# Optimization experiments

Hardware: AMD Instinct MI355X
Metric: run time of the kernel (lower is better)

Reference implementation:

```python
import jax, jax.numpy as jnp
import numpy as np
from jax import lax

DN = ('NCHW', 'OIHW', 'NCHW')

def _conv(x, w, b):
    y = lax.conv_general_dilated(x, w, (1, 1), 'SAME', dimension_numbers=DN)
    return y + b[None, :, None, None]

def setup_inputs() -> dict:
    key = jax.random.key(0)
    ks = jax.random.split(key, 11)
    B, C, H, W = 8, 16, 64, 64
    hid, K = 128, 8192
    s = 0.02
    return {
        'x': jax.random.normal(ks[0], (B, C, H, W), jnp.float32),
        # encoder: Conv2d(C->hid,3x3), GELU, Conv2d(hid->hid,3x3), GELU
        'ew1': jax.random.normal(ks[1], (hid, C, 3, 3), jnp.float32) * s,
        'eb1': jnp.zeros((hid,), jnp.float32),
        'ew2': jax.random.normal(ks[2], (hid, hid, 3, 3), jnp.float32) * s,
        'eb2': jnp.zeros((hid,), jnp.float32),
        # codebook: Embedding(K, hid), init normal std=0.02
        'embed': jax.random.normal(ks[3], (K, hid), jnp.float32) * s,
        # decoder: Conv2d(hid->hid,3x3), GELU, Conv2d(hid->C,1x1), sigmoid
        'dw1': jax.random.normal(ks[4], (hid, hid, 3, 3), jnp.float32) * s,
        'db1': jnp.zeros((hid,), jnp.float32),
        'dw2': jax.random.normal(ks[5], (C, hid, 1, 1), jnp.float32) * s,
        'db2': jnp.zeros((C,), jnp.float32),
    }

def reference(x, ew1, eb1, ew2, eb2, embed, dw1, db1, dw2, db2):
    # --- encoder ---
    h = jax.nn.gelu(_conv(x, ew1, eb1), approximate=False)
    h = jax.nn.gelu(_conv(h, ew2, eb2), approximate=False)  # [B, D, H, W]
    B, D, H, W = h.shape
    flat = jnp.transpose(h, (0, 2, 3, 1)).reshape(B * H * W, D)  # [N, D]
    # --- VQ: pairwise sq-dist + argmin (no_grad in original) ---
    flat_ng = lax.stop_gradient(flat)
    d2 = (jnp.sum(flat_ng * flat_ng, axis=1, keepdims=True)
          - 2.0 * flat_ng @ embed.T
          + jnp.sum(embed * embed, axis=1)[None, :])  # [N, K]
    idx = jnp.argmin(d2, axis=1)  # [N]
    z = idx.reshape(B, H, W)
    q = embed[idx].reshape(B, H, W, D)  # gather
    # --- decoder ---
    qc = jnp.transpose(q, (0, 3, 1, 2))  # NCHW
    y = jax.nn.gelu(_conv(qc, dw1, db1), approximate=False)
    x_hat = jax.nn.sigmoid(_conv(y, dw2, db2))  # [B, C, H, W]
    return x_hat
```

## Files before the change

kernel.cpp:

```cpp
#include <hip/hip_runtime.h>

constexpr int B_ = 8, H_ = 64, W_ = 64, C0 = 16, D_ = 128, K_ = 8192;
constexpr int N_ = B_ * H_ * W_;

typedef __attribute__((ext_vector_type(8))) short short8;
typedef __attribute__((ext_vector_type(4))) float f32x4;

__device__ __forceinline__ float gelu_f(float x) {
    return 0.5f * x * (1.0f + erff(x * 0.70710678118654752440f));
}

__device__ __forceinline__ unsigned short f2bf(float f) {
    unsigned u = __float_as_uint(f);
    u += 0x7fffu + ((u >> 16) & 1u);
    return (unsigned short)(u >> 16);
}

__device__ __forceinline__ void gload_lds16(const void* g, void* l) {
    __builtin_amdgcn_global_load_lds(
        (const __attribute__((address_space(1))) unsigned int*)g,
        (__attribute__((address_space(3))) unsigned int*)l, 16, 0, 0);
}

__global__ __launch_bounds__(256) void prep_kernel(
    const float* __restrict__ x, const float* __restrict__ ew1,
    const float* __restrict__ ew2, const float* __restrict__ dw1,
    const float* __restrict__ embed, unsigned short* __restrict__ xtbf,
    unsigned short* __restrict__ wtbf2, unsigned short* __restrict__ wtbf3,
    float* __restrict__ e2n, unsigned short* __restrict__ embbf,
    unsigned short* __restrict__ wtb1b,
    unsigned long long* __restrict__ partial,
    unsigned short* __restrict__ embq) {
    int blk = blockIdx.x;
    int tid = threadIdx.x;
    if (blk < 2048) {
        int j = blk * 256 + tid;
        int c = j & 15, w = (j >> 4) & 63, h = (j >> 10) & 63, b = j >> 16;
        xtbf[j] = f2bf(x[(((b << 4) + c) << 12) + (h << 6) + w]);
    } else if (blk < 3200) {
        const float* src = (blk < 2624) ? ew2 : dw1;
        unsigned short* dst = (blk < 2624) ? wtbf2 : wtbf3;
        int i = (blk - ((blk < 2624) ? 2048 : 2624)) * 256 + tid;
        int ci = i & 127, co = (i >> 7) & 127, t = i >> 14;
        dst[i] = f2bf(src[(co * 128 + ci) * 9 + t]);
    } else if (blk < 3232) {
        int k = (blk - 3200) * 256 + tid;
        const float4* e4 = (const float4*)(embed + (size_t)k * 128);
        float s = 0.0f;
#pragma unroll 8
        for (int i = 0; i < 32; ++i) {
            float4 v = e4[i];
            s += v.x * v.x + v.y * v.y + v.z * v.z + v.w * v.w;
        }
        e2n[k] = -0.5f * s;
    } else if (blk < 4256) {
        int i = (blk - 3232) * 256 + tid;
        float4 v = ((const float4*)embed)[i];
        uint2 o;
        o.x = (unsigned)f2bf(v.x) | ((unsigned)f2bf(v.y) << 16);
        o.y = (unsigned)f2bf(v.z) | ((unsigned)f2bf(v.w) << 16);
        ((uint2*)embbf)[i] = o;
    } else if (blk < 4336) {
        int i = (blk - 4256) * 256 + tid;
        int co = i / 160, kk = i % 160;
        float v = 0.0f;
        if (kk < 144) {
            int t = kk >> 4, ci = kk & 15;
            v = ew1[(co * 16 + ci) * 9 + t];
        }
        wtb1b[i] = f2bf(v);
    } else if (blk < 4464) {
        int i = (blk - 4336) * 256 + tid;
        partial[i] = 0ULL;
    } else {
        int s = (blk - 4464) * 256 + tid;
        int T = s >> 10;
        int rem = s & 1023;
        int kk = rem >> 8, nsp = (rem >> 6) & 3, q = (rem >> 4) & 3,
            r = rem & 15;
        int code = T * 64 + nsp * 16 + r;
        int d0 = kk * 32 + q * 8;
        const float* ep = embed + (size_t)code * 128 + d0;
        unsigned short* op = embq + (size_t)s * 8;
#pragma unroll
        for (int e = 0; e < 8; ++e) op[e] = f2bf(ep[e]);
    }
}

__global__ __launch_bounds__(256, 2) void conv1_mfma_kernel(
    const unsigned short* __restrict__ xtbf,
    const unsigned short* __restrict__ wtb1b,
    const float* __restrict__ bias,
    unsigned short* __restrict__ out) {
    constexpr int LDA = 168;
    __shared__ __align__(16) unsigned short As[64 * LDA];
    int tid = threadIdx.x;
    int wv = tid >> 6, lane = tid & 63;
    int r = lane & 15, q = lane >> 4;
    int h0 = blockIdx.x & 63, b = blockIdx.x >> 6;

    short8 bf1[5][2];
#pragma unroll
    for (int k = 0; k < 5; ++k)
#pragma unroll
        for (int ns = 0; ns < 2; ++ns)
            bf1[k][ns] = *(const short8*)(wtb1b + (wv * 32 + ns * 16 + r) * 160 +
                                          k * 32 + q * 8);

#pragma unroll
    for (int j = 0; j < 5; ++j) {
        int s = tid + j * 256;
        if (s < 1152) {
            int px = s / 18, rem = s % 18;
            int t = rem >> 1, half = rem & 1;
            int hh = h0 + t / 3 - 1, ww = px + t % 3 - 1;
            float4 v = make_float4(0.f, 0.f, 0.f, 0.f);
            if ((unsigned)hh < 64u && (unsigned)ww < 64u)
                v = *(const float4*)(xtbf + (((b * 64 + hh) * 64 + ww) << 4) +
                                     half * 8);
            *(float4*)(As + px * LDA + t * 16 + half * 8) = v;
        } else {
            int z = s - 1152;
            int px = z >> 1, half = z & 1;
            *(float4*)(As + px * LDA + 144 + half * 8) =
                make_float4(0.f, 0.f, 0.f, 0.f);
        }
    }
    __syncthreads();

    f32x4 acc[4][2];
#pragma unroll
    for (int ms = 0; ms < 4; ++ms)
#pragma unroll
        for (int ns = 0; ns < 2; ++ns) acc[ms][ns] = (f32x4){0.f, 0.f, 0.f, 0.f};

#pragma unroll
    for (int k = 0; k < 5; ++k) {
        short8 af[4];
#pragma unroll
        for (int ms = 0; ms < 4; ++ms)
            af[ms] = *(const short8*)(As + (ms * 16 + r) * LDA + k * 32 + q * 8);
#pragma unroll
        for (int ms = 0; ms < 4; ++ms)
#pragma unroll
            for (int ns = 0; ns < 2; ++ns)
                acc[ms][ns] = __builtin_amdgcn_mfma_f32_16x16x32_bf16(
                    af[ms], bf1[k][ns], acc[ms][ns], 0, 0, 0);
    }

#pragma unroll
    for (int ns = 0; ns < 2; ++ns) {
        int co = wv * 32 + ns * 16 + r;
        float bv = bias[co];
#pragma unroll
        for (int ms = 0; ms < 4; ++ms)
#pragma unroll
            for (int rg = 0; rg < 4; ++rg) {
                int px = ms * 16 + q * 4 + rg;
                int pix = (b * 64 + h0) * 64 + px;
                out[(size_t)pix * 128 + co] = f2bf(gelu_f(acc[ms][ns][rg] + bv));
            }
    }
}

template <bool OUT_BF16, bool GATHER, bool FUSE>
__global__ __launch_bounds__(256, 2) void conv3x3_mfma_kernel(
    const unsigned short* __restrict__ in,
    const unsigned long long* __restrict__ gidx,
    const unsigned short* __restrict__ wtb,
    const float* __restrict__ bias,
    const float* __restrict__ w2,
    const float* __restrict__ b2,
    void* __restrict__ out_) {
    constexpr int LDC = 136;
    __shared__ __align__(16) unsigned short As[3 * 66 * LDC];
    __shared__ __align__(16) float ws2[FUSE ? 2048 : 4];
    int tid = threadIdx.x;
    int wv = tid >> 6, lane = tid & 63;
    int r = lane & 15, q = lane >> 4;
    int h0 = blockIdx.x & 63, b = blockIdx.x >> 6;

    constexpr int NJ = FUSE ? 15 : 13;
    for (int j = 0; j < NJ; ++j) {
        int s = tid + j * 256;
        if (s < 3168) {
            int col = s >> 4, chunk = s & 15;
            int ry = col / 66, cx = col % 66;
            int hh = h0 - 1 + ry, ww = cx - 1;
            float4 v = make_float4(0.f, 0.f, 0.f, 0.f);
            if ((unsigned)hh < 64u && (unsigned)ww < 64u) {
                int pix = (b * 64 + hh) * 64 + ww;
                const unsigned short* src;
                if (GATHER) {
                    int k = 8191 - (int)(unsigned)(gidx[pix] & 0xFFFFFFFFu);
                    src = in + (size_t)k * 128;
                } else {
                    src = in + (size_t)pix * 128;
                }
                v = *(const float4*)(src + chunk * 8);
            }
            *(float4*)(As + col * LDC + chunk * 8) = v;
        } else if (FUSE && s < 3680) {
            int i = s - 3168;
            ((float4*)ws2)[i] = ((const float4*)w2)[i];
        }
    }
    __syncthreads();

    f32x4 acc[4][2];
#pragma unroll
    for (int ms = 0; ms < 4; ++ms)
#pragma unroll
        for (int ns = 0; ns < 2; ++ns) acc[ms][ns] = (f32x4){0.f, 0.f, 0.f, 0.f};

    const unsigned short* wbase = wtb + (wv * 32 + r) * 128 + q * 8;
    short8 bfp[2][2];
    bfp[0][0] = *(const short8*)(wbase);
    bfp[0][1] = *(const short8*)(wbase + 2048);
    int gcur = 0;
    for (int t = 0; t < 9; ++t) {
        int dy = t / 3, dx = t % 3;
#pragma unroll
        for (int k = 0; k < 4; ++k) {
            int cur = gcur & 1, nxt = cur ^ 1;
            if (gcur < 35) {
                int g1 = gcur + 1;
                int t1 = g1 >> 2, k1 = g1 & 3;
                const unsigned short* wp = wbase + t1 * 16384 + k1 * 32;
                bfp[nxt][0] = *(const short8*)(wp);
                bfp[nxt][1] = *(const short8*)(wp + 2048);
            }
            short8 af[4];
#pragma unroll
            for (int ms = 0; ms < 4; ++ms) {
                int col = dy * 66 + ms * 16 + r + dx;
                af[ms] = *(const short8*)(As + col * LDC + k * 32 + q * 8);
            }
#pragma unroll
            for (int ms = 0; ms < 4; ++ms)
#pragma unroll
                for (int ns = 0; ns < 2; ++ns)
                    acc[ms][ns] = __builtin_amdgcn_mfma_f32_16x16x32_bf16(
                        af[ms], bfp[cur][ns], acc[ms][ns], 0, 0, 0);
            ++gcur;
        }
    }

    if (!FUSE) {
#pragma unroll
        for (int ns = 0; ns < 2; ++ns) {
            int co = wv * 32 + ns * 16 + r;
            float bv = bias[co];
#pragma unroll
            for (int ms = 0; ms < 4; ++ms)
#pragma unroll
                for (int rg = 0; rg < 4; ++rg) {
                    int px = ms * 16 + q * 4 + rg;
                    int pix = (b * 64 + h0) * 64 + px;
                    float g = gelu_f(acc[ms][ns][rg] + bv);
                    if (OUT_BF16)
                        ((unsigned short*)out_)[(size_t)pix * 128 + co] = f2bf(g);
                    else
                        ((float*)out_)[(size_t)pix * 128 + co] = g;
                }
        }
    } else {
        __syncthreads();
        float* gbuf = (float*)As;
#pragma unroll
        for (int ns = 0; ns < 2; ++ns) {
            int co = wv * 32 + ns * 16 + r;
            float bv = bias[co];
#pragma unroll
            for (int ms = 0; ms < 4; ++ms)
#pragma unroll
                for (int rg = 0; rg < 4; ++rg) {
                    int px = ms * 16 + q * 4 + rg;
                    gbuf[px * 130 + co] = gelu_f(acc[ms][ns][rg] + bv);
                }
        }
        __syncthreads();
        int w_ = tid & 63, c0 = (tid >> 6) * 4;
        float a4[4] = {b2[c0], b2[c0 + 1], b2[c0 + 2], b2[c0 + 3]};
#pragma unroll 1
        for (int ci = 0; ci < 128; ci += 2) {
            float2 yv = *(const float2*)&gbuf[w_ * 130 + ci];
#pragma unroll
            for (int jc = 0; jc < 4; ++jc) {
                float2 wv2 = *(const float2*)&ws2[(c0 + jc) * 128 + ci];
                a4[jc] += yv.x * wv2.x + yv.y * wv2.y;
            }
        }
        float* outp = (float*)out_;
#pragma unroll
        for (int jc = 0; jc < 4; ++jc) {
            float v = 1.0f / (1.0f + expf(-a4[jc]));
            outp[(((size_t)b * 16 + c0 + jc) * 64 + h0) * 64 + w_] = v;
        }
    }
}

__global__ __launch_bounds__(256, 2) void vq_mfma_kernel(
    const unsigned short* __restrict__ flatbf,
    const unsigned short* __restrict__ embq,
    const float* __restrict__ e2n,
    unsigned long long* __restrict__ partial) {
    __shared__ __align__(16) unsigned short Bs[2][8192];
    int tid = threadIdx.x;
    int wv = tid >> 6, lane = tid & 63;
    int r = lane & 15, q = lane >> 4;
    int p_h = wv & 1;
    int c_s = wv >> 1;
    int half = blockIdx.x & 1;
    int m0 = (blockIdx.x >> 1) * 64;
    int kbase = half * 4096;
    int t0 = half * 64;

    short8 af[4][2];
#pragma unroll
    for (int kk = 0; kk < 4; ++kk)
#pragma unroll
        for (int ms = 0; ms < 2; ++ms)
            af[kk][ms] = *(const short8*)(
                flatbf + (size_t)(m0 + p_h * 32 + ms * 16 + r) * 128 +
                kk * 32 + q * 8);

    const float* e2p = e2n + kbase + c_s * 32 + r;
    float e2a = e2p[0], e2b = e2p[16];
    float e2nx0 = 0.f, e2nx1 = 0.f;

    {
        const unsigned short* src = embq + (size_t)t0 * 8192;
#pragma unroll
        for (int j = 0; j < 4; ++j) {
            int o = (j * 4 + wv) * 512;
            gload_lds16(src + o + lane * 8, &Bs[0][o]);
        }
    }

    float best[2][4];
#pragma unroll
    for (int ms = 0; ms < 2; ++ms)
#pragma unroll
        for (int rg = 0; rg < 4; ++rg) best[ms][rg] = -3.4e38f;

    __syncthreads();

    f32x4 acc[2][2];
#pragma unroll
    for (int ms = 0; ms < 2; ++ms) {
        acc[ms][0] = (f32x4){e2a, e2a, e2a, e2a};
        acc[ms][1] = (f32x4){e2b, e2b, e2b, e2b};
    }

    int cur = 0;
#pragma unroll 1
    for (int it = 0; it < 64; ++it) {
        if (it < 63) {
            const unsigned short* src = embq + (size_t)(t0 + it + 1) * 8192;
            unsigned short* dst = &Bs[cur ^ 1][0];
#pragma unroll
            for (int j = 0; j < 4; ++j) {
                int o = (j * 4 + wv) * 512;
                gload_lds16(src + o + lane * 8, dst + o);
            }
            e2nx0 = e2p[(it + 1) * 64];
            e2nx1 = e2p[(it + 1) * 64 + 16];
        }
        const unsigned short* bb = &Bs[cur][0];
#pragma unroll
        for (int kk = 0; kk < 4; ++kk) {
            short8 bf0 = *(const short8*)(bb + kk * 2048 + (c_s * 2) * 512 +
                                          q * 128 + r * 8);
            short8 bf1 = *(const short8*)(bb + kk * 2048 + (c_s * 2 + 1) * 512 +
                                          q * 128 + r * 8);
#pragma unroll
            for (int ms = 0; ms < 2; ++ms) {
                acc[ms][0] = __builtin_amdgcn_mfma_f32_16x16x32_bf16(
                    af[kk][ms], bf0, acc[ms][0], 0, 0, 0);
                acc[ms][1] = __builtin_amdgcn_mfma_f32_16x16x32_bf16(
                    af[kk][ms], bf1, acc[ms][1], 0, 0, 0);
            }
        }
        unsigned kb = (unsigned)(2047 - ((it & 31) * 64 + c_s * 32 + r));
#pragma unroll
        for (int ms = 0; ms < 2; ++ms)
#pragma unroll
            for (int rg = 0; rg < 4; ++rg) {
                float u0 = __uint_as_float(
                    (__float_as_uint(acc[ms][0][rg]) & 0xFFFFF800u) | kb);
                float u1 = __uint_as_float(
                    (__float_as_uint(acc[ms][1][rg]) & 0xFFFFF800u) |
                    (kb - 16u));
                best[ms][rg] = fmaxf(best[ms][rg], fmaxf(u0, u1));
            }
        if ((it & 31) == 31) {
#pragma unroll
            for (int ms = 0; ms < 2; ++ms)
#pragma unroll
                for (int rg = 0; rg < 4; ++rg) {
                    float v = best[ms][rg];
#pragma unroll
                    for (int m = 1; m < 16; m <<= 1)
                        v = fmaxf(v, __shfl_xor(v, m));
                    if (r == 0) {
                        unsigned bits = __float_as_uint(v);
                        int cand = 2047 - (int)(bits & 2047u);
                        int code = kbase + (it >> 5) * 2048 + cand;
                        unsigned sb = (bits & 0x80000000u) ? ~bits
                                                           : (bits | 0x80000000u);
                        unsigned long long packed =
                            ((unsigned long long)sb << 32) |
                            (unsigned)(8191 - code);
                        atomicMax(
                            partial + m0 + p_h * 32 + ms * 16 + q * 4 + rg,
                            packed);
                    }
                    best[ms][rg] = -3.4e38f;
                }
        }
        if (it < 63) {
#pragma unroll
            for (int ms = 0; ms < 2; ++ms) {
                acc[ms][0] = (f32x4){e2nx0, e2nx0, e2nx0, e2nx0};
                acc[ms][1] = (f32x4){e2nx1, e2nx1, e2nx1, e2nx1};
            }
        }
        __syncthreads();
        cur ^= 1;
    }
}

extern "C" void kernel_launch(void* const* d_in, const int* in_sizes, int n_in,
                              void* d_out, int out_size, void* d_ws,
                              size_t ws_size, hipStream_t stream) {
    const float* x = (const float*)d_in[0];
    const float* ew1 = (const float*)d_in[1];
    const float* eb1 = (const float*)d_in[2];
    const float* ew2 = (const float*)d_in[3];
    const float* eb2 = (const float*)d_in[4];
    const float* embed = (const float*)d_in[5];
    const float* dw1 = (const float*)d_in[6];
    const float* db1 = (const float*)d_in[7];
    const float* dw2 = (const float*)d_in[8];
    const float* db2 = (const float*)d_in[9];
    float* out = (float*)d_out;

    float* e2n = (float*)d_ws;
    unsigned long long* partial =
        (unsigned long long*)(e2n + 8192);
    unsigned short* xtbf = (unsigned short*)(partial + 32768);
    unsigned short* wtb1b = xtbf + 524288;
    unsigned short* wtbf2 = wtb1b + 20480;
    unsigned short* wtbf3 = wtbf2 + 147456;
    unsigned short* embbf = wtbf3 + 147456;
    unsigned short* abf = embbf + 1048576;
    unsigned short* flatbf = abf + 4194304;
    unsigned short* embq = flatbf + 4194304;

    prep_kernel<<<4976, 256, 0, stream>>>(x, ew1, ew2, dw1, embed, xtbf, wtbf2,
                                          wtbf3, e2n, embbf, wtb1b, partial,
                                          embq);
    conv1_mfma_kernel<<<512, 256, 0, stream>>>(xtbf, wtb1b, eb1, abf);
    conv3x3_mfma_kernel<true, false, false><<<512, 256, 0, stream>>>(
        abf, nullptr, wtbf2, eb2, nullptr, nullptr, flatbf);
    vq_mfma_kernel<<<1024, 256, 0, stream>>>(flatbf, embq, e2n, partial);
    conv3x3_mfma_kernel<false, true, true><<<512, 256, 0, stream>>>(
        embbf, partial, wtbf3, db1, dw2, db2, out);
}
```

Measured before the change: 222.7 us.

## Split 3x3 convs across output-channel halves and unfuse 1x1 decoder conv

The 3x3 conv kernels now launch twice as many blocks, each computing 64 output channels instead of 128. Each wave preloads all 36 of its weight fragments into registers instead of double-buffering them from global memory. The fused 1x1 conv and sigmoid epilogue moves into a separate dec2_kernel, which reads an fp32 intermediate written to workspace. This raises parallelism and removes weight-load latency from the MMA loop. In exchange, each input tile is loaded twice, register use rises, and an extra global round-trip for the fp32 intermediate plus an extra launch are added.

```diff
diff --git a/kernel.cpp b/kernel.cpp
--- a/kernel.cpp
+++ b/kernel.cpp
@@ -163,25 +163,31 @@
     }
 }
 
-template <bool OUT_BF16, bool GATHER, bool FUSE>
-__global__ __launch_bounds__(256, 2) void conv3x3_mfma_kernel(
+template <bool GATHER, bool OUT_F32>
+__global__ __launch_bounds__(256, 2) void conv3x3_w64_kernel(
     const unsigned short* __restrict__ in,
     const unsigned long long* __restrict__ gidx,
     const unsigned short* __restrict__ wtb,
     const float* __restrict__ bias,
-    const float* __restrict__ w2,
-    const float* __restrict__ b2,
     void* __restrict__ out_) {
     constexpr int LDC = 136;
     __shared__ __align__(16) unsigned short As[3 * 66 * LDC];
-    __shared__ __align__(16) float ws2[FUSE ? 2048 : 4];
     int tid = threadIdx.x;
     int wv = tid >> 6, lane = tid & 63;
     int r = lane & 15, q = lane >> 4;
-    int h0 = blockIdx.x & 63, b = blockIdx.x >> 6;
-
-    constexpr int NJ = FUSE ? 15 : 13;
-    for (int j = 0; j < NJ; ++j) {
+    int h0 = blockIdx.x & 63, b = (blockIdx.x >> 6) & 7;
+    int coh = blockIdx.x >> 9;
+    int co = coh * 64 + wv * 16 + r;
+
+    short8 wfr[9][4];
+#pragma unroll
+    for (int t = 0; t < 9; ++t)
+#pragma unroll
+        for (int k = 0; k < 4; ++k)
+            wfr[t][k] = *(const short8*)(wtb + t * 16384 + co * 128 + k * 32 +
+                                         q * 8);
+
+    for (int j = 0; j < 13; ++j) {
         int s = tid + j * 256;
         if (s < 3168) {
             int col = s >> 4, chunk = s & 15;
@@ -200,36 +206,19 @@
                 v = *(const float4*)(src + chunk * 8);
             }
             *(float4*)(As + col * LDC + chunk * 8) = v;
-        } else if (FUSE && s < 3680) {
-            int i = s - 3168;
-            ((float4*)ws2)[i] = ((const float4*)w2)[i];
         }
     }
     __syncthreads();
 
-    f32x4 acc[4][2];
-#pragma unroll
-    for (int ms = 0; ms < 4; ++ms)
-#pragma unroll
-        for (int ns = 0; ns < 2; ++ns) acc[ms][ns] = (f32x4){0.f, 0.f, 0.f, 0.f};
-
-    const unsigned short* wbase = wtb + (wv * 32 + r) * 128 + q * 8;
-    short8 bfp[2][2];
-    bfp[0][0] = *(const short8*)(wbase);
-    bfp[0][1] = *(const short8*)(wbase + 2048);
-    int gcur = 0;
+    f32x4 acc[4];
+#pragma unroll
+    for (int ms = 0; ms < 4; ++ms) acc[ms] = (f32x4){0.f, 0.f, 0.f, 0.f};
+
+#pragma unroll
     for (int t = 0; t < 9; ++t) {
         int dy = t / 3, dx = t % 3;
 #pragma unroll
         for (int k = 0; k < 4; ++k) {
-            int cur = gcur & 1, nxt = cur ^ 1;
-            if (gcur < 35) {
-                int g1 = gcur + 1;
-                int t1 = g1 >> 2, k1 = g1 & 3;
-                const unsigned short* wp = wbase + t1 * 16384 + k1 * 32;
-                bfp[nxt][0] = *(const short8*)(wp);
-                bfp[nxt][1] = *(const short8*)(wp + 2048);
-            }
             short8 af[4];
 #pragma unroll
             for (int ms = 0; ms < 4; ++ms) {
@@ -238,65 +227,63 @@
             }
 #pragma unroll
             for (int ms = 0; ms < 4; ++ms)
-#pragma unroll
-                for (int ns = 0; ns < 2; ++ns)
-                    acc[ms][ns] = __builtin_amdgcn_mfma_f32_16x16x32_bf16(
-                        af[ms], bfp[cur][ns], acc[ms][ns], 0, 0, 0);
-            ++gcur;
-        }
-    }
-
-    if (!FUSE) {
-#pragma unroll
-        for (int ns = 0; ns < 2; ++ns) {
-            int co = wv * 32 + ns * 16 + r;
-            float bv = bias[co];
-#pragma unroll
-            for (int ms = 0; ms < 4; ++ms)
-#pragma unroll
-                for (int rg = 0; rg < 4; ++rg) {
-                    int px = ms * 16 + q * 4 + rg;
-                    int pix = (b * 64 + h0) * 64 + px;
-                    float g = gelu_f(acc[ms][ns][rg] + bv);
-                    if (OUT_BF16)
-                        ((unsigned short*)out_)[(size_t)pix * 128 + co] = f2bf(g);
-                    else
-                        ((float*)out_)[(size_t)pix * 128 + co] = g;
-                }
-        }
-    } else {
-        __syncthreads();
-        float* gbuf = (float*)As;
-#pragma unroll
-        for (int ns = 0; ns < 2; ++ns) {
-            int co = wv * 32 + ns * 16 + r;
-            float bv = bias[co];
-#pragma unroll
-            for (int ms = 0; ms < 4; ++ms)
-#pragma unroll
-                for (int rg = 0; rg < 4; ++rg) {
-                    int px = ms * 16 + q * 4 + rg;
-                    gbuf[px * 130 + co] = gelu_f(acc[ms][ns][rg] + bv);
-                }
-        }
-        __syncthreads();
-        int w_ = tid & 63, c0 = (tid >> 6) * 4;
-        float a4[4] = {b2[c0], b2[c0 + 1], b2[c0 + 2], b2[c0 + 3]};
+                acc[ms] = __builtin_amdgcn_mfma_f32_16x16x32_bf16(
+                    af[ms], wfr[t][k], acc[ms], 0, 0, 0);
+        }
+    }
+
+    float bv = bias[co];
+#pragma unroll
+    for (int ms = 0; ms < 4; ++ms)
+#pragma unroll
+        for (int rg = 0; rg < 4; ++rg) {
+            int px = ms * 16 + q * 4 + rg;
+            int pix = (b * 64 + h0) * 64 + px;
+            float g = gelu_f(acc[ms][rg] + bv);
+            if (OUT_F32)
+                ((float*)out_)[(size_t)pix * 128 + co] = g;
+            else
+                ((unsigned short*)out_)[(size_t)pix * 128 + co] = f2bf(g);
+        }
+}
+
+__global__ __launch_bounds__(256, 2) void dec2_kernel(
+    const float* __restrict__ y,
+    const float* __restrict__ w2,
+    const float* __restrict__ b2,
+    float* __restrict__ out) {
+    __shared__ float yb[64 * 130];
+    __shared__ float ws2[2048];
+    int tid = threadIdx.x;
+    int h0 = blockIdx.x & 63, b = blockIdx.x >> 6;
+    const float4* ysrc = (const float4*)(y + (size_t)((b * 64 + h0) * 64) * 128);
+#pragma unroll
+    for (int j = 0; j < 8; ++j) {
+        int s = tid + j * 256;
+        int px = s >> 5, c4 = s & 31;
+        *(float4*)&yb[px * 130 + c4 * 4] = ysrc[s];
+    }
+#pragma unroll
+    for (int j = 0; j < 2; ++j) {
+        int s = tid + j * 256;
+        ((float4*)ws2)[s] = ((const float4*)w2)[s];
+    }
+    __syncthreads();
+    int w_ = tid & 63, c0 = (tid >> 6) * 4;
+    float a4[4] = {b2[c0], b2[c0 + 1], b2[c0 + 2], b2[c0 + 3]};
 #pragma unroll 1
-        for (int ci = 0; ci < 128; ci += 2) {
-            float2 yv = *(const float2*)&gbuf[w_ * 130 + ci];
-#pragma unroll
-            for (int jc = 0; jc < 4; ++jc) {
-                float2 wv2 = *(const float2*)&ws2[(c0 + jc) * 128 + ci];
-                a4[jc] += yv.x * wv2.x + yv.y * wv2.y;
-            }
-        }
-        float* outp = (float*)out_;
+    for (int ci = 0; ci < 128; ci += 2) {
+        float2 yv = *(const float2*)&yb[w_ * 130 + ci];
 #pragma unroll
         for (int jc = 0; jc < 4; ++jc) {
-            float v = 1.0f / (1.0f + expf(-a4[jc]));
-            outp[(((size_t)b * 16 + c0 + jc) * 64 + h0) * 64 + w_] = v;
-        }
+            float2 wv2 = *(const float2*)&ws2[(c0 + jc) * 128 + ci];
+            a4[jc] += yv.x * wv2.x + yv.y * wv2.y;
+        }
+    }
+#pragma unroll
+    for (int jc = 0; jc < 4; ++jc) {
+        float v = 1.0f / (1.0f + expf(-a4[jc]));
+        out[(((size_t)b * 16 + c0 + jc) * 64 + h0) * 64 + w_] = v;
     }
 }
 
@@ -457,14 +444,16 @@
     unsigned short* abf = embbf + 1048576;
     unsigned short* flatbf = abf + 4194304;
     unsigned short* embq = flatbf + 4194304;
+    float* yf = (float*)abf;
 
     prep_kernel<<<4976, 256, 0, stream>>>(x, ew1, ew2, dw1, embed, xtbf, wtbf2,
                                           wtbf3, e2n, embbf, wtb1b, partial,
                                           embq);
     conv1_mfma_kernel<<<512, 256, 0, stream>>>(xtbf, wtb1b, eb1, abf);
-    conv3x3_mfma_kernel<true, false, false><<<512, 256, 0, stream>>>(
-        abf, nullptr, wtbf2, eb2, nullptr, nullptr, flatbf);
+    conv3x3_w64_kernel<false, false><<<1024, 256, 0, stream>>>(
+        abf, nullptr, wtbf2, eb2, flatbf);
     vq_mfma_kernel<<<1024, 256, 0, stream>>>(flatbf, embq, e2n, partial);
-    conv3x3_mfma_kernel<false, true, true><<<512, 256, 0, stream>>>(
-        embbf, partial, wtbf3, db1, dw2, db2, out);
-}
+    conv3x3_w64_kernel<true, true><<<1024, 256, 0, stream>>>(
+        embbf, partial, wtbf3, db1, yf);
+    dec2_kernel<<<512, 256, 0, stream>>>(yf, dw2, db2, out);
+}
```

New measurement: 246.6 us. 1.11x slower.
